# Performance work log

Hardware: AMD Instinct MI355X
Metric: run time of the kernel (lower is better)

Reference implementation:

```python
import jax, jax.numpy as jnp
import numpy as np

N_NODES = 100000
N_EDGES = 1600000
N_HOPS = 3
D_FEAT = 128
D_HID = 256
NUM_GRAPHS = 64


def setup_inputs() -> dict:
    key = jax.random.key(0)
    ks = jax.random.split(key, 8)
    x = jax.random.normal(ks[0], (N_NODES, D_FEAT), dtype=jnp.float32)
    edge_index = jax.random.randint(ks[1], (N_HOPS, 2, N_EDGES), 0, N_NODES, dtype=jnp.int64)
    edge_weight = jax.random.uniform(ks[2], (N_HOPS, N_EDGES), dtype=jnp.float32)
    batch = jnp.sort(jax.random.randint(ks[3], (N_NODES,), 0, NUM_GRAPHS, dtype=jnp.int64))
    w1 = jax.random.normal(ks[4], (D_FEAT, D_HID), dtype=jnp.float32) * (1.0 / np.sqrt(D_FEAT))
    b1 = jnp.zeros((D_HID,), dtype=jnp.float32)
    w2 = jax.random.normal(ks[5], (D_HID, D_FEAT), dtype=jnp.float32) * (1.0 / np.sqrt(D_HID))
    b2 = jnp.zeros((D_FEAT,), dtype=jnp.float32)
    prop_w = jnp.ones((N_HOPS + 1,), dtype=jnp.float32)
    return {"x": x, "edge_index": edge_index, "edge_weight": edge_weight,
            "batch": batch, "w1": w1, "b1": b1, "w2": w2, "b2": b2, "prop_w": prop_w}


def reference(x, edge_index, edge_weight, batch, w1, b1, w2, b2, prop_w):
    n = x.shape[0]
    # MLP: dropout is identity in eval mode
    h = jax.nn.relu(x @ w1 + b1)          # [N, hid]
    h = h @ w2 + b2                        # [N, feat]
    # prop_weight: weighted sum over hops; hop i uses edge_index[layers[i]-1]
    acc = prop_w[0] * h
    for i in range(edge_index.shape[0]):
        src = edge_index[i, 0]             # x_j source nodes
        dst = edge_index[i, 1]             # aggregation targets
        msg = edge_weight[i][:, None] * h[src]              # [E, feat]
        agg = jax.ops.segment_sum(msg, dst, num_segments=n)  # [N, feat]
        acc = acc + prop_w[i + 1] * agg
    # sum over hop dim already folded into acc; global_add_pool over graphs
    pooled = jax.ops.segment_sum(acc, batch, num_segments=NUM_GRAPHS)  # [G, feat]
    # original returns log_softmax of pooled features (lin3 output is unused)
    return jax.nn.log_softmax(pooled, axis=1)
```

## Files before the change

kernel.cpp:

```cpp
#include <hip/hip_runtime.h>
#include <hip/hip_bf16.h>


#define N_NODES 100000
#define N_EDGES 1600000
#define N_HOPS 3
#define D_HID 256
#define N_GRAPHS 64

#define CHUNK 32
#define NCHUNK 3125
#define FG 512

#define NB 625
#define RB 160
#define NSH 4
#define CAP 2400
#define SGRID 500
#define SB 1024
#define I4PB 2400
#define NI4H 400000
#define STAGE_W 11475

#define CT_OFF    0u
#define BU8_OFF   0u
#define REC_OFF   12800000u
#define SPART_OFF REC_OFF
#define SMALL_OFF 36800000u
#define CUR_OFF   SMALL_OFF
#define TGR_OFF   (SMALL_OFF + 16384u)
#define SSUM_OFF  (SMALL_OFF + 32768u)
#define W1P_OFF   (SMALL_OFF + 131072u)

typedef __attribute__((ext_vector_type(4))) float f32x4;
typedef __attribute__((ext_vector_type(8))) short s16x8;
typedef __attribute__((ext_vector_type(4))) int i32x4;
typedef __attribute__((ext_vector_type(4))) float fv4;

__device__ __forceinline__ unsigned short f2bf_rne(float f) {
    union { float f; unsigned u; } v; v.f = f;
    unsigned r = v.u + 0x7FFFu + ((v.u >> 16) & 1u);
    return (unsigned short)(r >> 16);
}
__device__ __forceinline__ float bf2f(unsigned short s) {
    union { float f; unsigned u; } v; v.u = ((unsigned)s) << 16;
    return v.f;
}
__device__ __forceinline__ unsigned pk_rne(float lo, float hi) {
    return ((unsigned)f2bf_rne(hi) << 16) | (unsigned)f2bf_rne(lo);
}

__global__ __launch_bounds__(256) void prep_kernel(const float* __restrict__ w1,
                                                   unsigned short* __restrict__ w1p,
                                                   const int* __restrict__ batch,
                                                   unsigned char* __restrict__ bu8) {
    if (blockIdx.x < 16) {
        int f = blockIdx.x * 256 + threadIdx.x;
        int t = f >> 4, fr = f & 15, nt = fr >> 2, ks = fr & 3;
        int w = t >> 6, l = t & 63, q = l >> 4, c = l & 15;
        s16x8 v;
#pragma unroll
        for (int j = 0; j < 8; j++)
            v[j] = (short)f2bf_rne(w1[(size_t)(32 * ks + 8 * q + j) * 256 + w * 64 + 16 * nt + c]);
        *(s16x8*)&w1p[(size_t)f * 8] = v;
    } else {
        int i = (blockIdx.x - 16) * 1024 + threadIdx.x * 4;
        if (i < N_NODES) {
            int4 v = *(const int4*)&batch[i];
            uchar4 o;
            o.x = (unsigned char)v.x; o.y = (unsigned char)v.y;
            o.z = (unsigned char)v.z; o.w = (unsigned char)v.w;
            *(uchar4*)&bu8[i] = o;
        }
    }
}

__global__ __launch_bounds__(SB) void scatter_kernel(
    const int* __restrict__ ei, const float* __restrict__ ew,
    const unsigned char* __restrict__ bu8, const float* __restrict__ pw,
    unsigned* __restrict__ cursors, unsigned* __restrict__ records) {
    __shared__ unsigned cnt[NB], basearr[NB], lbase[NB], ccnt[NB];
    __shared__ unsigned wtot[16];
    __shared__ unsigned stage[STAGE_W];
    const int tid = threadIdx.x;
    const int lane = tid & 63, wid = tid >> 6;
    const int sh = blockIdx.x & (NSH - 1);
    const int i40 = blockIdx.x * I4PB;

    if (tid < NB) cnt[tid] = 0u;
    __syncthreads();

    const float pw1 = pw[1], pw2 = pw[2], pw3 = pw[3];

    unsigned rec[12], bkt[12];
#pragma unroll
    for (int k = 0; k < 3; k++) {
        int idx = tid + k * SB;
        if (idx < I4PB) {
            int i4 = i40 + idx;
            unsigned hop = (unsigned)i4 / NI4H;
            int r4 = i4 - (int)hop * NI4H;
            const i32x4* sp4 = (const i32x4*)(ei + (size_t)hop * 2 * N_EDGES);
            i32x4 s = __builtin_nontemporal_load(sp4 + r4);
            i32x4 d = __builtin_nontemporal_load(sp4 + NI4H + r4);
            fv4 wv = __builtin_nontemporal_load((const fv4*)(ew + (size_t)hop * N_EDGES) + r4);
            float pwh = hop == 0 ? pw1 : (hop == 1 ? pw2 : pw3);
#pragma unroll
            for (int j = 0; j < 4; j++) {
                unsigned b = (unsigned)s[j] / RB;
                bkt[k * 4 + j] = b;
                rec[k * 4 + j] = ((unsigned)f2bf_rne(pwh * wv[j]) << 16) |
                                 (unsigned)(((unsigned)s[j] - b * RB) * 64 + (unsigned)bu8[d[j]]);
                atomicAdd(&cnt[b], 1u);
            }
        } else {
#pragma unroll
            for (int j = 0; j < 4; j++) bkt[k * 4 + j] = 0xFFFFFFFFu;
        }
    }
    __syncthreads();

    unsigned pcv = 0;
    if (tid < NB) {
        unsigned cc = cnt[tid];
        ccnt[tid] = cc;
        pcv = (cc + 3u) & ~3u;
        basearr[tid] = pcv ? atomicAdd(&cursors[sh * NB + tid], pcv) : 0u;
        cnt[tid] = 0u;
    }
    unsigned inc = pcv;
#pragma unroll
    for (int d = 1; d < 64; d <<= 1) {
        unsigned u = __shfl_up(inc, d, 64);
        if (lane >= d) inc += u;
    }
    if (lane == 63) wtot[wid] = inc;
    __syncthreads();
    if (tid < 16) {
        unsigned wv = wtot[tid];
        unsigned winc = wv;
#pragma unroll
        for (int d = 1; d < 16; d <<= 1) {
            unsigned u = __shfl_up(winc, d, 16);
            if ((tid & 15) >= d) winc += u;
        }
        wtot[tid] = winc - wv;
    }
    __syncthreads();
    if (tid < NB) {
        unsigned lb = inc - pcv + wtot[wid];
        lbase[tid] = lb;
        for (unsigned i = ccnt[tid]; i < pcv; i++) stage[lb + i] = 0u;
    }
    __syncthreads();

#pragma unroll
    for (int k = 0; k < 12; k++) {
        if (bkt[k] != 0xFFFFFFFFu) {
            unsigned o = atomicAdd(&cnt[bkt[k]], 1u);
            stage[lbase[bkt[k]] + o] = rec[k];
        }
    }
    __syncthreads();

    if (tid < NB) {
        unsigned pc = (ccnt[tid] + 3u) & ~3u;
        unsigned lb = lbase[tid];
        unsigned* dst = records + ((size_t)sh * NB + tid) * CAP + basearr[tid];
        for (unsigned i = 0; i < pc; i += 4) {
            uint4 v = *(const uint4*)&stage[lb + i];
            *(uint4*)&dst[i] = v;
        }
    }
}

__global__ __launch_bounds__(512) void phaseB_kernel(
    const int* __restrict__ batch, const float* __restrict__ pw,
    const unsigned* __restrict__ cursors, const unsigned* __restrict__ records,
    unsigned short* __restrict__ ct, float* __restrict__ tgr) {
    __shared__ float tile[RB * 65];
    const int tid = threadIdx.x;
    const int b = blockIdx.x;

    for (int i = tid; i < RB * 65; i += 512) tile[i] = 0.f;

    unsigned ncur[NSH];
#pragma unroll
    for (int sh = 0; sh < NSH; sh++) ncur[sh] = cursors[sh * NB + b];

    __syncthreads();

    if (tid < RB) atomicAdd(&tile[tid * 65 + batch[b * RB + tid]], pw[0]);

    for (int sh = 0; sh < NSH; sh++) {
        unsigned n = ncur[sh];
        const unsigned* rp = records + ((size_t)sh * NB + b) * CAP;
        unsigned n4 = n >> 2;
        for (unsigned i = tid; i < n4; i += 512) {
            uint4 r4 = *(const uint4*)(rp + 4 * i);
            unsigned m0 = r4.x & 0x3FFFu, m1 = r4.y & 0x3FFFu;
            unsigned m2 = r4.z & 0x3FFFu, m3 = r4.w & 0x3FFFu;
            atomicAdd(&tile[m0 + (m0 >> 6)], bf2f((unsigned short)(r4.x >> 16)));
            atomicAdd(&tile[m1 + (m1 >> 6)], bf2f((unsigned short)(r4.y >> 16)));
            atomicAdd(&tile[m2 + (m2 >> 6)], bf2f((unsigned short)(r4.z >> 16)));
            atomicAdd(&tile[m3 + (m3 >> 6)], bf2f((unsigned short)(r4.w >> 16)));
        }
        unsigned i = 4 * n4 + tid;
        if (i < n) {
            unsigned r = rp[i];
            unsigned m = r & 0x3FFFu;
            atomicAdd(&tile[m + (m >> 6)], bf2f((unsigned short)(r >> 16)));
        }
    }
    __syncthreads();

    if (tid < 256) {
        const int gt = tid >> 6, l = tid & 63, q = l >> 4, c = l & 15;
        for (int cc = 0; cc < 5; cc++) {
            s16x8 v;
#pragma unroll
            for (int j = 0; j < 8; j++)
                v[j] = (short)f2bf_rne(tile[(cc * 32 + 8 * q + j) * 65 + 16 * gt + c]);
            *(s16x8*)&ct[(((size_t)(b * 5 + cc) * 4 + gt) * 64 + l) * 8] = v;
        }
    }
    if (tid < 64) {
        float sum = 0.f;
        for (int s = 0; s < RB; s++) sum += tile[s * 65 + tid];
        atomicAdd(&tgr[(b & 63) * 64 + tid], sum);
    }
}

__global__ __launch_bounds__(256, 2) void fused_kernel(
    const float* __restrict__ x,
    const unsigned short* __restrict__ w1p,
    const float* __restrict__ b1,
    const unsigned short* __restrict__ ct,
    unsigned short* __restrict__ s_part) {

    __shared__ __align__(16) unsigned short Ut[256 * 40];
    __shared__ __align__(16) unsigned short x_lds[32 * 136];
    __shared__ __align__(16) unsigned short ct_lds[2048];

    const int tid = threadIdx.x;
    const int w = tid >> 6, l = tid & 63, q = l >> 4, c = l & 15;
    const int wcol = w * 64;
    const int sr = tid >> 3, sk = (tid & 7) * 16;

    s16x8 w1f[4][4];
    {
        const s16x8* wp = (const s16x8*)(w1p + (size_t)tid * 128);
#pragma unroll
        for (int nt = 0; nt < 4; nt++)
#pragma unroll
            for (int ks = 0; ks < 4; ks++)
                w1f[nt][ks] = wp[nt * 4 + ks];
    }

    float bias[4];
#pragma unroll
    for (int nt = 0; nt < 4; nt++) bias[nt] = b1[wcol + 16 * nt + c];

    f32x4 sacc[4][4];
#pragma unroll
    for (int gt = 0; gt < 4; gt++)
#pragma unroll
        for (int nt = 0; nt < 4; nt++) sacc[gt][nt] = (f32x4)0.f;

    uint4 xp0, xp1;
    s16x8 ctp;

#define PREF(CI)                                                              \
    {                                                                         \
        const float4* p = (const float4*)&x[(size_t)((CI) * 32 + sr) * 128 + sk]; \
        float4 v0 = p[0], v1 = p[1], v2 = p[2], v3 = p[3];                    \
        xp0.x = pk_rne(v0.x, v0.y); xp0.y = pk_rne(v0.z, v0.w);               \
        xp0.z = pk_rne(v1.x, v1.y); xp0.w = pk_rne(v1.z, v1.w);               \
        xp1.x = pk_rne(v2.x, v2.y); xp1.y = pk_rne(v2.z, v2.w);               \
        xp1.z = pk_rne(v3.x, v3.y); xp1.w = pk_rne(v3.z, v3.w);               \
        ctp = *(const s16x8*)&ct[(size_t)(CI) * 2048 + tid * 8];              \
    }

    int ci = blockIdx.x;
    if (ci < NCHUNK) PREF(ci);

    for (; ci < NCHUNK; ci += FG) {
        *(uint4*)&x_lds[sr * 136 + sk] = xp0;
        *(uint4*)&x_lds[sr * 136 + sk + 8] = xp1;
        *(s16x8*)&ct_lds[tid * 8] = ctp;
        __syncthreads();

        s16x8 af[2][4], ctf[4];
#pragma unroll
        for (int mt = 0; mt < 2; mt++)
#pragma unroll
            for (int ks = 0; ks < 4; ks++)
                af[mt][ks] = *(const s16x8*)&x_lds[(16 * mt + c) * 136 + 32 * ks + 8 * q];
#pragma unroll
        for (int gt = 0; gt < 4; gt++)
            ctf[gt] = *(const s16x8*)&ct_lds[(gt * 64 + l) * 8];
        __syncthreads();

        if (ci + FG < NCHUNK) PREF(ci + FG);

        f32x4 u[2][4];
#pragma unroll
        for (int mt = 0; mt < 2; mt++)
#pragma unroll
            for (int nt = 0; nt < 4; nt++) {
                f32x4 a; a[0] = a[1] = a[2] = a[3] = bias[nt];
                u[mt][nt] = a;
            }
#pragma unroll
        for (int ks = 0; ks < 4; ks++)
#pragma unroll
            for (int mt = 0; mt < 2; mt++)
#pragma unroll
                for (int nt = 0; nt < 4; nt++)
                    u[mt][nt] = __builtin_amdgcn_mfma_f32_16x16x32_bf16(
                        af[mt][ks], w1f[nt][ks], u[mt][nt], 0, 0, 0);

#pragma unroll
        for (int mt = 0; mt < 2; mt++)
#pragma unroll
            for (int nt = 0; nt < 4; nt++) {
                f32x4 v = u[mt][nt];
                uint2 d;
                d.x = pk_rne(fmaxf(v[0], 0.f), fmaxf(v[1], 0.f));
                d.y = pk_rne(fmaxf(v[2], 0.f), fmaxf(v[3], 0.f));
                *(uint2*)&Ut[(wcol + 16 * nt + c) * 40 + 16 * mt + 4 * q] = d;
            }

#pragma unroll
        for (int nt = 0; nt < 4; nt++) {
            s16x8 uf = *(const s16x8*)&Ut[(wcol + 16 * nt + c) * 40 + 8 * q];
#pragma unroll
            for (int gt = 0; gt < 4; gt++)
                sacc[gt][nt] = __builtin_amdgcn_mfma_f32_16x16x32_bf16(
                    ctf[gt], uf, sacc[gt][nt], 0, 0, 0);
        }
    }
#undef PREF

    unsigned short* my = s_part + (size_t)blockIdx.x * (64 * 256);
#pragma unroll
    for (int gt = 0; gt < 4; gt++)
#pragma unroll
        for (int nt = 0; nt < 4; nt++)
#pragma unroll
            for (int r = 0; r < 4; r++)
                my[(16 * gt + 4 * q + r) * 256 + wcol + 16 * nt + c] =
                    f2bf_rne(sacc[gt][nt][r]);
}

__global__ __launch_bounds__(256) void reduce_kernel(const unsigned short* __restrict__ s_part,
                                                     float* __restrict__ s_sum) {
    __shared__ float red[4][64];
    const int l = threadIdx.x & 63, p = threadIdx.x >> 6;
    const int e = blockIdx.x * 64 + l;
    float a0 = 0.f, a1 = 0.f, a2 = 0.f, a3 = 0.f;
    for (int b = p * (FG / 4); b < (p + 1) * (FG / 4); b += 4) {
        a0 += bf2f(s_part[(size_t)(b + 0) * 16384 + e]);
        a1 += bf2f(s_part[(size_t)(b + 1) * 16384 + e]);
        a2 += bf2f(s_part[(size_t)(b + 2) * 16384 + e]);
        a3 += bf2f(s_part[(size_t)(b + 3) * 16384 + e]);
    }
    red[p][l] = (a0 + a1) + (a2 + a3);
    __syncthreads();
    if (p == 0) s_sum[e] = (red[0][l] + red[1][l]) + (red[2][l] + red[3][l]);
}

__global__ void finalize_kernel(const float* __restrict__ s,
                                const float* __restrict__ tgr,
                                const float* __restrict__ w2,
                                const float* __restrict__ b2,
                                float* __restrict__ out) {
    __shared__ float red[128];
    __shared__ float tgs;
    const int g = blockIdx.x;
    const int f = threadIdx.x;

    if (f < 64) {
        float v = tgr[f * 64 + g];
        for (int off = 32; off; off >>= 1) v += __shfl_down(v, off, 64);
        if (f == 0) tgs = v;
    }
    __syncthreads();

    float acc = tgs * b2[f];
    for (int k = 0; k < D_HID; k++)
        acc += s[(size_t)g * 256 + k] * w2[(size_t)k * 128 + f];

    red[f] = acc;
    __syncthreads();
    for (int off = 64; off > 0; off >>= 1) {
        if (f < off) red[f] = fmaxf(red[f], red[f + off]);
        __syncthreads();
    }
    float mx = red[0];
    __syncthreads();
    red[f] = expf(acc - mx);
    __syncthreads();
    for (int off = 64; off > 0; off >>= 1) {
        if (f < off) red[f] += red[f + off];
        __syncthreads();
    }
    float lse = logf(red[0]);
    out[(size_t)g * 128 + f] = acc - mx - lse;
}

extern "C" void kernel_launch(void* const* d_in, const int* in_sizes, int n_in,
                              void* d_out, int out_size, void* d_ws, size_t ws_size,
                              hipStream_t stream) {
    const float* x     = (const float*)d_in[0];
    const int*   ei    = (const int*)d_in[1];
    const float* ew    = (const float*)d_in[2];
    const int*   batch = (const int*)d_in[3];
    const float* w1    = (const float*)d_in[4];
    const float* b1    = (const float*)d_in[5];
    const float* w2    = (const float*)d_in[6];
    const float* b2    = (const float*)d_in[7];
    const float* pw    = (const float*)d_in[8];
    float* out = (float*)d_out;

    unsigned short* ctp     = (unsigned short*)((char*)d_ws + CT_OFF);
    unsigned char*  bu8     = (unsigned char*)((char*)d_ws + BU8_OFF);
    unsigned*       records = (unsigned*)((char*)d_ws + REC_OFF);
    unsigned short* s_part  = (unsigned short*)((char*)d_ws + SPART_OFF);
    unsigned*       cursors = (unsigned*)((char*)d_ws + CUR_OFF);
    float*          tgrp    = (float*)((char*)d_ws + TGR_OFF);
    float*          s_sum   = (float*)((char*)d_ws + SSUM_OFF);
    unsigned short* w1pp    = (unsigned short*)((char*)d_ws + W1P_OFF);

    hipMemsetAsync(cursors, 0, NSH * NB * sizeof(unsigned), stream);
    hipMemsetAsync(tgrp, 0, 64 * 64 * sizeof(float), stream);

    prep_kernel<<<dim3(114), 256, 0, stream>>>(w1, w1pp, batch, bu8);
    scatter_kernel<<<dim3(SGRID), SB, 0, stream>>>(
        ei, ew, bu8, pw, cursors, records);
    phaseB_kernel<<<dim3(NB), 512, 0, stream>>>(batch, pw, cursors, records, ctp, tgrp);
    fused_kernel<<<dim3(FG), 256, 0, stream>>>(x, w1pp, b1, ctp, s_part);
    reduce_kernel<<<dim3(256), 256, 0, stream>>>(s_part, s_sum);
    finalize_kernel<<<dim3(64), 128, 0, stream>>>(s_sum, tgrp, w2, b2, out);
}
```

Measured before the change: 237.5 us.

## Replace global atomic bucket cursors with per-block contiguous record runs and offset table

The scatter kernel no longer reserves space in per-shard bucket arrays with global atomics. Each block now writes its whole bucket-sorted staging buffer as one contiguous, coalesced run, plus a per-(block,bucket) offset/count table. phaseB then has each of 500 threads walk one source block's segment for its bucket. This removes the cursor memset and the global atomics and turns scattered stores into streaming stores. The cost is that phaseB reads many small, short, uncoalesced segments with one thread per segment, which can leave its load work imbalanced.

After: 231.2 us. 1.03x faster.

```diff
diff --git a/kernel.cpp b/kernel.cpp
--- a/kernel.cpp
+++ b/kernel.cpp
@@ -14,21 +14,20 @@
 
 #define NB 625
 #define RB 160
-#define NSH 4
-#define CAP 2400
 #define SGRID 500
 #define SB 1024
 #define I4PB 2400
 #define NI4H 400000
 #define STAGE_W 11475
+#define RSTRIDE 11776
 
 #define CT_OFF    0u
 #define BU8_OFF   0u
 #define REC_OFF   12800000u
 #define SPART_OFF REC_OFF
-#define SMALL_OFF 36800000u
-#define CUR_OFF   SMALL_OFF
-#define TGR_OFF   (SMALL_OFF + 16384u)
+#define OFFS_OFF  36500000u
+#define SMALL_OFF 40000000u
+#define TGR_OFF   SMALL_OFF
 #define SSUM_OFF  (SMALL_OFF + 32768u)
 #define W1P_OFF   (SMALL_OFF + 131072u)
 
@@ -78,13 +77,13 @@
 __global__ __launch_bounds__(SB) void scatter_kernel(
     const int* __restrict__ ei, const float* __restrict__ ew,
     const unsigned char* __restrict__ bu8, const float* __restrict__ pw,
-    unsigned* __restrict__ cursors, unsigned* __restrict__ records) {
-    __shared__ unsigned cnt[NB], basearr[NB], lbase[NB], ccnt[NB];
+    unsigned* __restrict__ offs, unsigned* __restrict__ records) {
+    __shared__ unsigned cnt[NB], lbase[NB], ccnt[NB];
     __shared__ unsigned wtot[16];
+    __shared__ unsigned tot;
     __shared__ unsigned stage[STAGE_W];
     const int tid = threadIdx.x;
     const int lane = tid & 63, wid = tid >> 6;
-    const int sh = blockIdx.x & (NSH - 1);
     const int i40 = blockIdx.x * I4PB;
 
     if (tid < NB) cnt[tid] = 0u;
@@ -125,7 +124,6 @@
         unsigned cc = cnt[tid];
         ccnt[tid] = cc;
         pcv = (cc + 3u) & ~3u;
-        basearr[tid] = pcv ? atomicAdd(&cursors[sh * NB + tid], pcv) : 0u;
         cnt[tid] = 0u;
     }
     unsigned inc = pcv;
@@ -150,6 +148,8 @@
     if (tid < NB) {
         unsigned lb = inc - pcv + wtot[wid];
         lbase[tid] = lb;
+        offs[(size_t)blockIdx.x * NB + tid] = (pcv << 16) | lb;
+        if (tid == NB - 1) tot = lb + pcv;
         for (unsigned i = ccnt[tid]; i < pcv; i++) stage[lb + i] = 0u;
     }
     __syncthreads();
@@ -163,53 +163,38 @@
     }
     __syncthreads();
 
-    if (tid < NB) {
-        unsigned pc = (ccnt[tid] + 3u) & ~3u;
-        unsigned lb = lbase[tid];
-        unsigned* dst = records + ((size_t)sh * NB + tid) * CAP + basearr[tid];
-        for (unsigned i = 0; i < pc; i += 4) {
-            uint4 v = *(const uint4*)&stage[lb + i];
-            *(uint4*)&dst[i] = v;
-        }
+    unsigned total = tot;
+    unsigned* dst = records + (size_t)blockIdx.x * RSTRIDE;
+    for (unsigned i = tid * 4; i < total; i += SB * 4) {
+        *(uint4*)&dst[i] = *(const uint4*)&stage[i];
     }
 }
 
 __global__ __launch_bounds__(512) void phaseB_kernel(
     const int* __restrict__ batch, const float* __restrict__ pw,
-    const unsigned* __restrict__ cursors, const unsigned* __restrict__ records,
+    const unsigned* __restrict__ offs, const unsigned* __restrict__ records,
     unsigned short* __restrict__ ct, float* __restrict__ tgr) {
     __shared__ float tile[RB * 65];
     const int tid = threadIdx.x;
     const int b = blockIdx.x;
 
     for (int i = tid; i < RB * 65; i += 512) tile[i] = 0.f;
-
-    unsigned ncur[NSH];
-#pragma unroll
-    for (int sh = 0; sh < NSH; sh++) ncur[sh] = cursors[sh * NB + b];
-
     __syncthreads();
 
     if (tid < RB) atomicAdd(&tile[tid * 65 + batch[b * RB + tid]], pw[0]);
 
-    for (int sh = 0; sh < NSH; sh++) {
-        unsigned n = ncur[sh];
-        const unsigned* rp = records + ((size_t)sh * NB + b) * CAP;
-        unsigned n4 = n >> 2;
-        for (unsigned i = tid; i < n4; i += 512) {
-            uint4 r4 = *(const uint4*)(rp + 4 * i);
+    if (tid < SGRID) {
+        unsigned w = offs[(size_t)tid * NB + b];
+        const unsigned* rp = records + (size_t)tid * RSTRIDE + (w & 0xFFFFu);
+        unsigned pc = w >> 16;
+        for (unsigned i = 0; i < pc; i += 4) {
+            uint4 r4 = *(const uint4*)(rp + i);
             unsigned m0 = r4.x & 0x3FFFu, m1 = r4.y & 0x3FFFu;
             unsigned m2 = r4.z & 0x3FFFu, m3 = r4.w & 0x3FFFu;
             atomicAdd(&tile[m0 + (m0 >> 6)], bf2f((unsigned short)(r4.x >> 16)));
             atomicAdd(&tile[m1 + (m1 >> 6)], bf2f((unsigned short)(r4.y >> 16)));
             atomicAdd(&tile[m2 + (m2 >> 6)], bf2f((unsigned short)(r4.z >> 16)));
             atomicAdd(&tile[m3 + (m3 >> 6)], bf2f((unsigned short)(r4.w >> 16)));
-        }
-        unsigned i = 4 * n4 + tid;
-        if (i < n) {
-            unsigned r = rp[i];
-            unsigned m = r & 0x3FFFu;
-            atomicAdd(&tile[m + (m >> 6)], bf2f((unsigned short)(r >> 16)));
         }
     }
     __syncthreads();
@@ -427,18 +412,17 @@
     unsigned char*  bu8     = (unsigned char*)((char*)d_ws + BU8_OFF);
     unsigned*       records = (unsigned*)((char*)d_ws + REC_OFF);
     unsigned short* s_part  = (unsigned short*)((char*)d_ws + SPART_OFF);
-    unsigned*       cursors = (unsigned*)((char*)d_ws + CUR_OFF);
+    unsigned*       offsp   = (unsigned*)((char*)d_ws + OFFS_OFF);
     float*          tgrp    = (float*)((char*)d_ws + TGR_OFF);
     float*          s_sum   = (float*)((char*)d_ws + SSUM_OFF);
     unsigned short* w1pp    = (unsigned short*)((char*)d_ws + W1P_OFF);
 
-    hipMemsetAsync(cursors, 0, NSH * NB * sizeof(unsigned), stream);
     hipMemsetAsync(tgrp, 0, 64 * 64 * sizeof(float), stream);
 
     prep_kernel<<<dim3(114), 256, 0, stream>>>(w1, w1pp, batch, bu8);
     scatter_kernel<<<dim3(SGRID), SB, 0, stream>>>(
-        ei, ew, bu8, pw, cursors, records);
-    phaseB_kernel<<<dim3(NB), 512, 0, stream>>>(batch, pw, cursors, records, ctp, tgrp);
+        ei, ew, bu8, pw, offsp, records);
+    phaseB_kernel<<<dim3(NB), 512, 0, stream>>>(batch, pw, offsp, records, ctp, tgrp);
     fused_kernel<<<dim3(FG), 256, 0, stream>>>(x, w1pp, b1, ctp, s_part);
     reduce_kernel<<<dim3(256), 256, 0, stream>>>(s_part, s_sum);
     finalize_kernel<<<dim3(64), 128, 0, stream>>>(s_sum, tgrp, w2, b2, out);
```
